# Optimization experiments

Measured on AMD Instinct MI355X. Metric: run time of the kernel, lower is better.

## Reference

```python
import jax, jax.numpy as jnp
import numpy as np

N = 100000      # nodes (dtype==2 subgraph)
E = 1600000     # edges
IN_DIM = 256
OUT_DIM = 64
FEAT_DIM = 64   # hard-coded by nn.Linear(64, out_dim) in dstfeat_fc


def setup_inputs() -> dict:
    key = jax.random.key(0)
    k1, k2, k3, k4, k5, k6 = jax.random.split(key, 6)
    h = jax.random.normal(k1, (N, IN_DIM), dtype=jnp.float32)
    feat = jax.random.normal(k2, (N, FEAT_DIM), dtype=jnp.float32)
    W_fc = jax.random.normal(k3, (OUT_DIM, IN_DIM), dtype=jnp.float32) * 0.05
    W_dst = jax.random.normal(k4, (OUT_DIM, FEAT_DIM), dtype=jnp.float32) * 0.05
    src = jax.random.randint(k5, (E,), 0, N, dtype=jnp.int64)
    dst = jax.random.randint(k6, (E,), 0, N, dtype=jnp.int64)
    return {"h": h, "feat": feat, "W_fc": W_fc, "W_dst": W_dst, "src": src, "dst": dst}


def reference(h, feat, W_fc, W_dst, src, dst):
    # node projections (done once per node, then gathered per edge)
    z = h @ W_fc.T            # [N, OUT]  (self.fc)
    df = feat @ W_dst.T       # [N, OUT]  (self.dstfeat_fc on dst 'feat')

    # per-edge attention logit: dot(z[src], dstfeat[dst])
    e = jnp.sum(z[src] * df[dst], axis=-1)          # [E]

    # segment softmax over incoming edges of each destination node
    emax = jax.ops.segment_max(e, dst, num_segments=N)
    emax = jnp.where(jnp.isfinite(emax), emax, 0.0)  # guard empty segments
    ex = jnp.exp(e - emax[dst])                      # [E]
    denom = jax.ops.segment_sum(ex, dst, num_segments=N)  # [N]

    # weighted neighbor aggregation: sum_e alpha_e * z[src_e] per dst
    num = jax.ops.segment_sum(ex[:, None] * z[src], dst, num_segments=N)  # [N, OUT]
    out = num / jnp.where(denom == 0, 1.0, denom)[:, None]
    return out
```

## Files before the change

### kernel.cpp

```cpp
#include <hip/hip_runtime.h>
#include <math.h>

typedef unsigned int uint32;
typedef __attribute__((ext_vector_type(8))) short bf16x8;
typedef __attribute__((ext_vector_type(4))) float f32x4;

__device__ __forceinline__ ushort f2bf(float f) {
  uint32 u = __builtin_bit_cast(uint32, f);
  uint32 r = (u + 0x7fff + ((u >> 16) & 1)) >> 16;
  return (ushort)r;
}
__device__ __forceinline__ float bf_lo(uint32 u) {
  return __builtin_bit_cast(float, u << 16);
}
__device__ __forceinline__ float bf_hi(uint32 u) {
  return __builtin_bit_cast(float, u & 0xffff0000u);
}

__global__ __launch_bounds__(256) void gemm_both(const float* __restrict__ h,
                                                 const float* __restrict__ feat,
                                                 const float* __restrict__ W_fc,
                                                 const float* __restrict__ W_dst,
                                                 ushort* __restrict__ zb,
                                                 float* __restrict__ df,
                                                 int M, int gsplit) {
  __shared__ __align__(16) ushort Ws[64 * 264];
  __shared__ __align__(16) ushort As[128 * 40];
  const bool second = (int)blockIdx.x >= gsplit;
  const float* __restrict__ A = second ? feat : h;
  const float* __restrict__ W = second ? W_dst : W_fc;
  const int K = second ? 64 : 256;
  const int bx = second ? (int)blockIdx.x - gsplit : (int)blockIdx.x;

  const int t = threadIdx.x;
  const int lane = t & 63;
  const int w = t >> 6;
  const int quad = lane >> 4;
  const int l16 = lane & 15;
  const int rBase = bx * 128;

  const int kq4 = K >> 2;
  for (int idx = t; idx < 64 * kq4; idx += 256) {
    int row = idx / kq4, kq = idx - row * kq4;
    float4 v = *(const float4*)(W + (size_t)row * K + kq * 4);
    ushort4 b;
    b.x = f2bf(v.x); b.y = f2bf(v.y); b.z = f2bf(v.z); b.w = f2bf(v.w);
    *(ushort4*)&Ws[row * 264 + kq * 4] = b;
  }

  f32x4 acc[2][4];
  #pragma unroll
  for (int i = 0; i < 2; ++i)
    #pragma unroll
    for (int n = 0; n < 4; ++n) acc[i][n] = (f32x4){0.f, 0.f, 0.f, 0.f};

  const int rStage = t >> 1;
  const int halfStage = t & 1;

  for (int kb = 0; kb < K; kb += 32) {
    {
      int gr = rBase + rStage;
      #pragma unroll
      for (int q = 0; q < 4; ++q) {
        int kk = kb + halfStage * 16 + q * 4;
        float4 v = make_float4(0.f, 0.f, 0.f, 0.f);
        if (gr < M) v = *(const float4*)(A + (size_t)gr * K + kk);
        ushort4 b;
        b.x = f2bf(v.x); b.y = f2bf(v.y); b.z = f2bf(v.z); b.w = f2bf(v.w);
        *(ushort4*)&As[rStage * 40 + halfStage * 16 + q * 4] = b;
      }
    }
    __syncthreads();

    bf16x8 afrag[2], bfrag[4];
    #pragma unroll
    for (int i = 0; i < 2; ++i)
      afrag[i] = *(const bf16x8*)&As[(w * 32 + i * 16 + l16) * 40 + quad * 8];
    #pragma unroll
    for (int n = 0; n < 4; ++n)
      bfrag[n] = *(const bf16x8*)&Ws[(n * 16 + l16) * 264 + kb + quad * 8];

    #pragma unroll
    for (int i = 0; i < 2; ++i)
      #pragma unroll
      for (int n = 0; n < 4; ++n)
        acc[i][n] = __builtin_amdgcn_mfma_f32_16x16x32_bf16(afrag[i], bfrag[n],
                                                            acc[i][n], 0, 0, 0);
    __syncthreads();
  }

  #pragma unroll
  for (int i = 0; i < 2; ++i)
    #pragma unroll
    for (int nt = 0; nt < 4; ++nt)
      #pragma unroll
      for (int r = 0; r < 4; ++r) {
        int row = rBase + w * 32 + i * 16 + quad * 4 + r;
        int col = nt * 16 + l16;
        if (row < M) {
          if (!second)
            zb[(size_t)row * 64 + col] = f2bf(acc[i][nt][r]);
          else
            df[(size_t)row * 64 + col] = acc[i][nt][r];
        }
      }
}

#define NBBITS 9
#define BKNODES 512
#define CH 4096
#define NBMAX 256

__global__ __launch_bounds__(256) void csr_count(const int* __restrict__ dst,
                                                 int* __restrict__ bCnt, int E, int NB) {
  __shared__ int lcnt[NBMAX];
  const int t = threadIdx.x;
  if (t < NB) lcnt[t] = 0;
  __syncthreads();
  const int c0 = blockIdx.x * CH, c1 = min(c0 + CH, E);
  for (int i = c0 + t; i < c1; i += 256) atomicAdd(&lcnt[dst[i] >> NBBITS], 1);
  __syncthreads();
  if (t < NB) {
    int c = lcnt[t];
    if (c) atomicAdd(&bCnt[t], c);
  }
}

__global__ __launch_bounds__(256) void csr_scan(const int* __restrict__ bCnt,
                                                int* __restrict__ bBase,
                                                int* __restrict__ bCursor,
                                                int* __restrict__ offsets,
                                                int NB, int N, int E) {
  __shared__ int wsum[4];
  const int t = threadIdx.x;
  const int lane = t & 63, wave = t >> 6;
  int x = (t < NB) ? bCnt[t] : 0;
  int inc = x;
  #pragma unroll
  for (int d = 1; d < 64; d <<= 1) {
    int o = __shfl_up(inc, d, 64);
    if (lane >= d) inc += o;
  }
  if (lane == 63) wsum[wave] = inc;
  __syncthreads();
  int wbase = 0;
  #pragma unroll
  for (int w = 0; w < 4; ++w)
    if (w < wave) wbase += wsum[w];
  int excl = wbase + inc - x;
  if (t < NB) {
    bBase[t] = excl;
    bCursor[t] = excl;
  }
  if (t == 0) {
    bBase[NB] = E;
    offsets[N] = E;
  }
}

__global__ __launch_bounds__(256) void csr_partition(const int* __restrict__ src,
                                                     const int* __restrict__ dst,
                                                     int* __restrict__ bCursor,
                                                     unsigned* __restrict__ packed,
                                                     int E, int NB) {
  __shared__ int lcnt[NBMAX];
  __shared__ int lbase[NBMAX];
  const int t = threadIdx.x;
  if (t < NB) lcnt[t] = 0;
  __syncthreads();
  const int c0 = blockIdx.x * CH, c1 = min(c0 + CH, E);
  for (int i = c0 + t; i < c1; i += 256) atomicAdd(&lcnt[dst[i] >> NBBITS], 1);
  __syncthreads();
  if (t < NB) {
    int c = lcnt[t];
    lbase[t] = c ? atomicAdd(&bCursor[t], c) : 0;
  }
  __syncthreads();
  for (int i = c0 + t; i < c1; i += 256) {
    int dv = dst[i];
    int b = dv >> NBBITS;
    int pos = atomicAdd(&lbase[b], 1);
    packed[pos] = ((unsigned)src[i] << NBBITS) | (unsigned)(dv & (BKNODES - 1));
  }
}

__global__ __launch_bounds__(256) void csr_finalize(const int* __restrict__ bBase,
                                                    const unsigned* __restrict__ packed,
                                                    int* __restrict__ edgeSrc,
                                                    int* __restrict__ offsets, int N) {
  __shared__ int sh[BKNODES];
  __shared__ int wsum[4];
  const int r = blockIdx.x;
  const int t = threadIdx.x;
  const int lane = t & 63, wave = t >> 6;
  const int base = bBase[r];
  const int endr = bBase[r + 1];
  for (int i = t; i < BKNODES; i += 256) sh[i] = 0;
  __syncthreads();
  for (int i = base + t; i < endr; i += 256)
    atomicAdd(&sh[packed[i] & (BKNODES - 1)], 1);
  __syncthreads();
  {
    int cA = sh[2 * t], cB = sh[2 * t + 1];
    int s = cA + cB;
    int inc = s;
    #pragma unroll
    for (int d = 1; d < 64; d <<= 1) {
      int o = __shfl_up(inc, d, 64);
      if (lane >= d) inc += o;
    }
    if (lane == 63) wsum[wave] = inc;
    __syncthreads();
    int wbase = 0;
    #pragma unroll
    for (int w = 0; w < 4; ++w)
      if (w < wave) wbase += wsum[w];
    int excl = wbase + inc - s;
    sh[2 * t] = base + excl;
    sh[2 * t + 1] = base + excl + cA;
  }
  __syncthreads();
  const int node0 = r << NBBITS;
  for (int k = t; k < BKNODES; k += 256) {
    int g = node0 + k;
    if (g < N) offsets[g] = sh[k];
  }
  __syncthreads();
  for (int i = base + t; i < endr; i += 256) {
    unsigned v = packed[i];
    int pos = atomicAdd(&sh[v & (BKNODES - 1)], 1);
    edgeSrc[pos] = (int)(v >> NBBITS);
  }
}

__global__ __launch_bounds__(256) void aggregate(const ushort* __restrict__ zb,
                                                 const float* __restrict__ df,
                                                 const int* __restrict__ offsets,
                                                 const int* __restrict__ edgeSrc,
                                                 float* __restrict__ out, int N) {
  int gwave = (blockIdx.x * blockDim.x + threadIdx.x) >> 6;
  int lane = threadIdx.x & 63;
  if (gwave >= N) return;
  const int d = __builtin_amdgcn_readfirstlane(gwave);
  const int g = lane >> 4;
  const int l16 = lane & 15;
  const int beg = offsets[d];
  const int end = offsets[d + 1];

  const float4 df4 = *(const float4*)(df + (size_t)d * 64 + l16 * 4);

  float m = -INFINITY, l = 0.f;
  float ax = 0.f, ay = 0.f, az = 0.f, aw = 0.f;

  for (int j0 = beg; j0 < end; j0 += 32) {
    const int nst = min(8, (end - j0 + 3) >> 2);
    uint2 zf[8];
    float ew[8];
    float bm = -INFINITY;

    #pragma unroll
    for (int st = 0; st < 8; ++st) {
      if (st < nst) {
        const int eidx = j0 + st * 4 + g;
        const bool act = eidx < end;
        int s = 0;
        if (act) s = edgeSrc[eidx];
        zf[st] = *(const uint2*)(zb + (size_t)s * 64 + l16 * 4);
        float p = bf_lo(zf[st].x) * df4.x;
        p = fmaf(bf_hi(zf[st].x), df4.y, p);
        p = fmaf(bf_lo(zf[st].y), df4.z, p);
        p = fmaf(bf_hi(zf[st].y), df4.w, p);
        p += __shfl_xor(p, 1, 64);
        p += __shfl_xor(p, 2, 64);
        p += __shfl_xor(p, 4, 64);
        p += __shfl_xor(p, 8, 64);
        ew[st] = act ? p : -INFINITY;
        bm = fmaxf(bm, ew[st]);
      }
    }
    bm = fmaxf(bm, __shfl_xor(bm, 16, 64));
    bm = fmaxf(bm, __shfl_xor(bm, 32, 64));

    const float nm = fmaxf(m, bm);
    const float alpha = __expf(m - nm);
    float sw = 0.f;
    #pragma unroll
    for (int st = 0; st < 8; ++st) {
      if (st < nst) {
        const float w = __expf(ew[st] - nm);
        ew[st] = w;
        sw += w;
      }
    }
    sw += __shfl_xor(sw, 16, 64);
    sw += __shfl_xor(sw, 32, 64);
    l = l * alpha + sw;
    m = nm;

    ax *= alpha; ay *= alpha; az *= alpha; aw *= alpha;
    #pragma unroll
    for (int st = 0; st < 8; ++st) {
      if (st < nst) {
        const float w = ew[st];
        ax = fmaf(w, bf_lo(zf[st].x), ax);
        ay = fmaf(w, bf_hi(zf[st].x), ay);
        az = fmaf(w, bf_lo(zf[st].y), az);
        aw = fmaf(w, bf_hi(zf[st].y), aw);
      }
    }
  }

  ax += __shfl_xor(ax, 16, 64); ax += __shfl_xor(ax, 32, 64);
  ay += __shfl_xor(ay, 16, 64); ay += __shfl_xor(ay, 32, 64);
  az += __shfl_xor(az, 16, 64); az += __shfl_xor(az, 32, 64);
  aw += __shfl_xor(aw, 16, 64); aw += __shfl_xor(aw, 32, 64);

  if (lane < 16) {
    const float inv = (l > 0.f) ? (1.f / l) : 0.f;
    float4 o;
    o.x = ax * inv; o.y = ay * inv; o.z = az * inv; o.w = aw * inv;
    *(float4*)(out + (size_t)d * 64 + l16 * 4) = o;
  }
}

extern "C" void kernel_launch(void* const* d_in, const int* in_sizes, int n_in,
                              void* d_out, int out_size, void* d_ws, size_t ws_size,
                              hipStream_t stream) {
  const float* h     = (const float*)d_in[0];
  const float* feat  = (const float*)d_in[1];
  const float* W_fc  = (const float*)d_in[2];
  const float* W_dst = (const float*)d_in[3];
  const int*   src   = (const int*)d_in[4];
  const int*   dst   = (const int*)d_in[5];
  float* out = (float*)d_out;

  const int N = in_sizes[1] / 64;
  const int E = in_sizes[4];

  const int NB = (N + BKNODES - 1) >> NBBITS;
  const int nChunks = (E + CH - 1) / CH;

  char* ws = (char*)d_ws;
  ushort* zb = (ushort*)ws;
  float* df = (float*)(zb + (size_t)N * 64);
  int* offsets = (int*)(df + (size_t)N * 64);
  int* edgeSrc = offsets + N + 1;
  int* bCnt = edgeSrc + E;
  int* bBase = bCnt + NB;
  int* bCursor = bBase + NB + 1;
  unsigned* packed = (unsigned*)d_out;

  hipMemsetAsync(bCnt, 0, sizeof(int) * (size_t)NB, stream);

  const int gsplit = (N + 127) / 128;
  gemm_both<<<gsplit * 2, 256, 0, stream>>>(h, feat, W_fc, W_dst, zb, df, N, gsplit);

  csr_count<<<nChunks, 256, 0, stream>>>(dst, bCnt, E, NB);
  csr_scan<<<1, 256, 0, stream>>>(bCnt, bBase, bCursor, offsets, NB, N, E);
  csr_partition<<<nChunks, 256, 0, stream>>>(src, dst, bCursor, packed, E, NB);
  csr_finalize<<<NB, 256, 0, stream>>>(bBase, packed, edgeSrc, offsets, N);

  aggregate<<<(N + 3) / 4, 256, 0, stream>>>(zb, df, offsets, edgeSrc, out, N);
}
```

Baseline: 358.2 us.

## Load GEMM A-fragments directly from global into registers, drop LDS staging

The projection GEMM no longer stages A tiles through shared memory with two barriers per k-step. Each lane now loads its own MFMA A-fragment rows straight from global memory, converts them to bf16 in registers, and issues the MFMAs. The kernel body is templated on K and output type so the loops are specialised, and launch bounds request 4 blocks per CU. In exchange, global loads become less coalesced (each lane reads 32 bytes per row) and there is no reuse through LDS. Clamping rows to M-1 keeps reads in bounds without a branch.

```diff
diff --git a/kernel.cpp b/kernel.cpp
--- a/kernel.cpp
+++ b/kernel.cpp
@@ -17,27 +17,19 @@
   return __builtin_bit_cast(float, u & 0xffff0000u);
 }
 
-__global__ __launch_bounds__(256) void gemm_both(const float* __restrict__ h,
-                                                 const float* __restrict__ feat,
-                                                 const float* __restrict__ W_fc,
-                                                 const float* __restrict__ W_dst,
-                                                 ushort* __restrict__ zb,
-                                                 float* __restrict__ df,
-                                                 int M, int gsplit) {
-  __shared__ __align__(16) ushort Ws[64 * 264];
-  __shared__ __align__(16) ushort As[128 * 40];
-  const bool second = (int)blockIdx.x >= gsplit;
-  const float* __restrict__ A = second ? feat : h;
-  const float* __restrict__ W = second ? W_dst : W_fc;
-  const int K = second ? 64 : 256;
-  const int bx = second ? (int)blockIdx.x - gsplit : (int)blockIdx.x;
-
+template <int K, bool BF16OUT>
+__device__ __forceinline__ void gemm_body(const float* __restrict__ A,
+                                          const float* __restrict__ W,
+                                          ushort* __restrict__ Cb,
+                                          float* __restrict__ C,
+                                          int M, int bx, ushort* Ws) {
   const int t = threadIdx.x;
   const int lane = t & 63;
   const int w = t >> 6;
   const int quad = lane >> 4;
   const int l16 = lane & 15;
   const int rBase = bx * 128;
+  const int WSTR = K + 8;
 
   const int kq4 = K >> 2;
   for (int idx = t; idx < 64 * kq4; idx += 256) {
@@ -45,8 +37,9 @@
     float4 v = *(const float4*)(W + (size_t)row * K + kq * 4);
     ushort4 b;
     b.x = f2bf(v.x); b.y = f2bf(v.y); b.z = f2bf(v.z); b.w = f2bf(v.w);
-    *(ushort4*)&Ws[row * 264 + kq * 4] = b;
-  }
+    *(ushort4*)&Ws[row * WSTR + kq * 4] = b;
+  }
+  __syncthreads();
 
   f32x4 acc[2][4];
   #pragma unroll
@@ -54,39 +47,37 @@
     #pragma unroll
     for (int n = 0; n < 4; ++n) acc[i][n] = (f32x4){0.f, 0.f, 0.f, 0.f};
 
-  const int rStage = t >> 1;
-  const int halfStage = t & 1;
-
+  const int r0 = min(rBase + w * 32 + l16, M - 1);
+  const int r1 = min(rBase + w * 32 + 16 + l16, M - 1);
+  const float* __restrict__ a0 = A + (size_t)r0 * K + quad * 8;
+  const float* __restrict__ a1 = A + (size_t)r1 * K + quad * 8;
+
+  #pragma unroll 2
   for (int kb = 0; kb < K; kb += 32) {
-    {
-      int gr = rBase + rStage;
-      #pragma unroll
-      for (int q = 0; q < 4; ++q) {
-        int kk = kb + halfStage * 16 + q * 4;
-        float4 v = make_float4(0.f, 0.f, 0.f, 0.f);
-        if (gr < M) v = *(const float4*)(A + (size_t)gr * K + kk);
-        ushort4 b;
-        b.x = f2bf(v.x); b.y = f2bf(v.y); b.z = f2bf(v.z); b.w = f2bf(v.w);
-        *(ushort4*)&As[rStage * 40 + halfStage * 16 + q * 4] = b;
-      }
-    }
-    __syncthreads();
-
-    bf16x8 afrag[2], bfrag[4];
-    #pragma unroll
-    for (int i = 0; i < 2; ++i)
-      afrag[i] = *(const bf16x8*)&As[(w * 32 + i * 16 + l16) * 40 + quad * 8];
+    float4 v00 = *(const float4*)(a0 + kb);
+    float4 v01 = *(const float4*)(a0 + kb + 4);
+    float4 v10 = *(const float4*)(a1 + kb);
+    float4 v11 = *(const float4*)(a1 + kb + 4);
+    bf16x8 af0, af1;
+    af0[0] = (short)f2bf(v00.x); af0[1] = (short)f2bf(v00.y);
+    af0[2] = (short)f2bf(v00.z); af0[3] = (short)f2bf(v00.w);
+    af0[4] = (short)f2bf(v01.x); af0[5] = (short)f2bf(v01.y);
+    af0[6] = (short)f2bf(v01.z); af0[7] = (short)f2bf(v01.w);
+    af1[0] = (short)f2bf(v10.x); af1[1] = (short)f2bf(v10.y);
+    af1[2] = (short)f2bf(v10.z); af1[3] = (short)f2bf(v10.w);
+    af1[4] = (short)f2bf(v11.x); af1[5] = (short)f2bf(v11.y);
+    af1[6] = (short)f2bf(v11.z); af1[7] = (short)f2bf(v11.w);
+
+    bf16x8 bfrag[4];
     #pragma unroll
     for (int n = 0; n < 4; ++n)
-      bfrag[n] = *(const bf16x8*)&Ws[(n * 16 + l16) * 264 + kb + quad * 8];
-
-    #pragma unroll
-    for (int i = 0; i < 2; ++i)
-      #pragma unroll
-      for (int n = 0; n < 4; ++n)
-        acc[i][n] = __builtin_amdgcn_mfma_f32_16x16x32_bf16(afrag[i], bfrag[n],
-                                                            acc[i][n], 0, 0, 0);
-    __syncthreads();
+      bfrag[n] = *(const bf16x8*)&Ws[(n * 16 + l16) * WSTR + kb + quad * 8];
+
+    #pragma unroll
+    for (int n = 0; n < 4; ++n) {
+      acc[0][n] = __builtin_amdgcn_mfma_f32_16x16x32_bf16(af0, bfrag[n], acc[0][n], 0, 0, 0);
+      acc[1][n] = __builtin_amdgcn_mfma_f32_16x16x32_bf16(af1, bfrag[n], acc[1][n], 0, 0, 0);
+    }
   }
 
   #pragma unroll
@@ -98,12 +89,26 @@
         int row = rBase + w * 32 + i * 16 + quad * 4 + r;
         int col = nt * 16 + l16;
         if (row < M) {
-          if (!second)
-            zb[(size_t)row * 64 + col] = f2bf(acc[i][nt][r]);
+          if (BF16OUT)
+            Cb[(size_t)row * 64 + col] = f2bf(acc[i][nt][r]);
           else
-            df[(size_t)row * 64 + col] = acc[i][nt][r];
+            C[(size_t)row * 64 + col] = acc[i][nt][r];
         }
       }
+}
+
+__global__ __launch_bounds__(256, 4) void gemm_both(const float* __restrict__ h,
+                                                    const float* __restrict__ feat,
+                                                    const float* __restrict__ W_fc,
+                                                    const float* __restrict__ W_dst,
+                                                    ushort* __restrict__ zb,
+                                                    float* __restrict__ df,
+                                                    int M, int gsplit) {
+  __shared__ __align__(16) ushort Ws[64 * 264];
+  if ((int)blockIdx.x < gsplit)
+    gemm_body<256, true>(h, W_fc, zb, nullptr, M, (int)blockIdx.x, Ws);
+  else
+    gemm_body<64, false>(feat, W_dst, nullptr, df, M, (int)blockIdx.x - gsplit, Ws);
 }
 
 #define NBBITS 9
```

New measurement: 350.9 us. 1.02x faster.
